# Kernel tuning notes

Hardware: AMD Instinct MI355X
Metric: run time of the kernel (lower is better)

## Reference

```python
import jax, jax.numpy as jnp
import numpy as np

BETA = 0.25  # commitment-loss weight


def setup_inputs() -> dict:
    key = jax.random.key(0)
    k1, k2 = jax.random.split(key)
    # x: [B, H, W, D] so that x.reshape(-1, D) groups per-pixel latent vectors
    x = jax.random.normal(k1, (32, 64, 64, 64), dtype=jnp.float32)
    # codebook: [D, K] as in the torch module (embedding_dim, num_embeddings)
    embedding = jax.random.normal(k2, (64, 1024), dtype=jnp.float32)
    return {"x": x, "embedding": embedding}


def reference(x, embedding):
    D, K = embedding.shape
    flat = x.reshape(-1, D)  # [N, D]
    # pairwise squared distances: ||z||^2 + ||e||^2 - 2 z.e  -> [N, K]
    distances = (
        jnp.sum(flat * flat, axis=1, keepdims=True)
        + jnp.sum(embedding * embedding, axis=0)
        - 2.0 * (flat @ embedding)
    )
    encoding_indices = jnp.argmin(distances, axis=1)  # [N]
    encodings = jax.nn.one_hot(encoding_indices, K, dtype=x.dtype)  # [N, K]
    # gather codewords (same math as encodings @ embedding.T, but O(N*D))
    quantized = jnp.take(embedding, encoding_indices, axis=1).T.reshape(x.shape)
    e_latent_loss = jnp.mean((jax.lax.stop_gradient(quantized) - x) ** 2)
    loss = BETA * e_latent_loss
    # straight-through estimator
    quantized_st = x + jax.lax.stop_gradient(quantized - x)
    avg_probs = jnp.mean(encodings, axis=0)
    perplexity = jnp.exp(-jnp.sum(avg_probs * jnp.log(avg_probs + 1e-10)))
    return quantized_st, loss, perplexity, encodings, encoding_indices
```

## Files before the change

### kernel.cpp

```cpp
#include <hip/hip_runtime.h>
#include <hip/hip_fp16.h>
#include <math.h>

#define NPIX    131072
#define DDIM    64
#define KCODE   1024
#define BETA    0.25f
#define EPS2    4e-3f
#define FIXCAP  2048
#define TAILROW 130944

#define Q_OFF    0
#define LOSS_OFF 8388608
#define PERP_OFF 8388609
#define ENC_OFF  8388610
#define IDX_OFF  142606338

#define TAIL_F     134086656
#define EHT_F      (TAIL_F + 2)
#define ELT_F      (TAIL_F + 32770)
#define FIXLIST_I  (TAIL_F + 65540)
#define FIXDELTA_F (TAIL_F + 69638)
#define FIXCOUNT_I (TAIL_F + 71688)


typedef _Float16 half8 __attribute__((ext_vector_type(8)));
typedef float    f32x4 __attribute__((ext_vector_type(4)));

__global__ void vq_prep(const float* __restrict__ emb, float* __restrict__ embT,
                        _Float16* __restrict__ eh, _Float16* __restrict__ el,
                        float* __restrict__ norms) {
    int b = blockIdx.x;
    if (b < 256) {
        int i = b * 256 + threadIdx.x;
        int d = i >> 10;
        int k = i & 1023;
        float v = emb[i];
        embT[k * DDIM + d] = v;
        _Float16 h = (_Float16)v;
        eh[k * DDIM + d] = h;
        el[k * DDIM + d] = (_Float16)(v - (float)h);
    } else {
        int k = (b - 256) * 256 + threadIdx.x;
        float s = 0.f;
        #pragma unroll 8
        for (int d = 0; d < DDIM; ++d) {
            float v = emb[d * KCODE + k];
            s = fmaf(v, v, s);
        }
        norms[k] = s;
    }
}

__global__ __launch_bounds__(256) void vq_argmin_fused(
        const float* __restrict__ x, const _Float16* __restrict__ eh,
        const _Float16* __restrict__ el, const float* __restrict__ norms,
        const float* __restrict__ embT, float* __restrict__ idxf,
        float* __restrict__ q, float* __restrict__ enc,
        int* __restrict__ hist, float* __restrict__ lossp,
        int* __restrict__ fixlist, int* __restrict__ fixcount) {
    __shared__ char lds_raw[33280];
    half8* EH8 = (half8*)lds_raw;
    half8* EL8 = (half8*)(lds_raw + 16384);
    float* NRM = (float*)(lds_raw + 32768);

    const int tid   = threadIdx.x;
    const int blkid = blockIdx.x;
    const int wave  = tid >> 6;
    const int lane  = tid & 63;
    const int lx = lane & 15;
    const int lk = lane >> 4;
    const int pixbase = blkid * 128 + wave * 32;

    half8 ah[2][2], al[2][2];
    float xp0 = 0.f, xp1 = 0.f;
    #pragma unroll
    for (int mt = 0; mt < 2; ++mt) {
        const float* xr = x + (size_t)(pixbase + mt * 16 + lx) * DDIM + lk * 8;
        float xps = 0.f;
        #pragma unroll
        for (int kh = 0; kh < 2; ++kh) {
            float4 v0 = *(const float4*)(xr + kh * 32);
            float4 v1 = *(const float4*)(xr + kh * 32 + 4);
            xps = fmaf(v0.x, v0.x, xps); xps = fmaf(v0.y, v0.y, xps);
            xps = fmaf(v0.z, v0.z, xps); xps = fmaf(v0.w, v0.w, xps);
            xps = fmaf(v1.x, v1.x, xps); xps = fmaf(v1.y, v1.y, xps);
            xps = fmaf(v1.z, v1.z, xps); xps = fmaf(v1.w, v1.w, xps);
            half8 hh, ll;
            float vv;
            vv = v0.x; hh[0] = (_Float16)vv; ll[0] = (_Float16)(vv - (float)hh[0]);
            vv = v0.y; hh[1] = (_Float16)vv; ll[1] = (_Float16)(vv - (float)hh[1]);
            vv = v0.z; hh[2] = (_Float16)vv; ll[2] = (_Float16)(vv - (float)hh[2]);
            vv = v0.w; hh[3] = (_Float16)vv; ll[3] = (_Float16)(vv - (float)hh[3]);
            vv = v1.x; hh[4] = (_Float16)vv; ll[4] = (_Float16)(vv - (float)hh[4]);
            vv = v1.y; hh[5] = (_Float16)vv; ll[5] = (_Float16)(vv - (float)hh[5]);
            vv = v1.z; hh[6] = (_Float16)vv; ll[6] = (_Float16)(vv - (float)hh[6]);
            vv = v1.w; hh[7] = (_Float16)vv; ll[7] = (_Float16)(vv - (float)hh[7]);
            ah[mt][kh] = hh;
            al[mt][kh] = ll;
        }
        if (mt == 0) xp0 = xps; else xp1 = xps;
    }
    float xn0 = xp0 + __shfl_xor(xp0, 16); xn0 += __shfl_xor(xn0, 32);
    float xn1 = xp1 + __shfl_xor(xp1, 16); xn1 += __shfl_xor(xn1, 32);

    float b1[2][4], b2[2][4];
    int   i1[2][4];
    #pragma unroll
    for (int mt = 0; mt < 2; ++mt)
        #pragma unroll
        for (int r = 0; r < 4; ++r) { b1[mt][r] = 3.4e38f; b2[mt][r] = 3.4e38f; i1[mt][r] = 0; }

    float* encB = enc + (size_t)blkid * 131072;
    f32x4* zb = (f32x4*)(encB + 2);

    #pragma unroll 1
    for (int t = 0; t < 8; ++t) {
        const int kbase = t * 128;
        __syncthreads();
        {
            const float4* sh = (const float4*)(eh + (size_t)kbase * DDIM);
            const float4* sl = (const float4*)(el + (size_t)kbase * DDIM);
            float4* dh = (float4*)EH8;
            float4* dl = (float4*)EL8;
            #pragma unroll
            for (int i = 0; i < 4; ++i) {
                int G = tid + i * 256;
                int code = G >> 3, g = G & 7;
                int sw = g ^ (code & 7);
                dh[code * 8 + sw] = sh[G];
                dl[code * 8 + sw] = sl[G];
            }
            if (tid < 128) NRM[tid] = norms[kbase + tid];
        }
        __syncthreads();

        #pragma unroll 1
        for (int c = 0; c < 8; ++c) {
            int code = c * 16 + lx;
            const half8* bhp = EH8 + code * 8;
            const half8* blp = EL8 + code * 8;
            int sw0 = lk ^ (code & 7);
            int sw1 = (lk + 4) ^ (code & 7);
            half8 bh0 = bhp[sw0], bh1 = bhp[sw1];
            half8 bl0 = blp[sw0], bl1 = blp[sw1];

            f32x4 acc0 = {0.f, 0.f, 0.f, 0.f};
            f32x4 acc1 = {0.f, 0.f, 0.f, 0.f};
            acc0 = __builtin_amdgcn_mfma_f32_16x16x32_f16(ah[0][0], bh0, acc0, 0, 0, 0);
            acc1 = __builtin_amdgcn_mfma_f32_16x16x32_f16(ah[1][0], bh0, acc1, 0, 0, 0);
            acc0 = __builtin_amdgcn_mfma_f32_16x16x32_f16(ah[0][1], bh1, acc0, 0, 0, 0);
            acc1 = __builtin_amdgcn_mfma_f32_16x16x32_f16(ah[1][1], bh1, acc1, 0, 0, 0);
            acc0 = __builtin_amdgcn_mfma_f32_16x16x32_f16(ah[0][0], bl0, acc0, 0, 0, 0);
            acc1 = __builtin_amdgcn_mfma_f32_16x16x32_f16(ah[1][0], bl0, acc1, 0, 0, 0);
            acc0 = __builtin_amdgcn_mfma_f32_16x16x32_f16(ah[0][1], bl1, acc0, 0, 0, 0);
            acc1 = __builtin_amdgcn_mfma_f32_16x16x32_f16(ah[1][1], bl1, acc1, 0, 0, 0);
            acc0 = __builtin_amdgcn_mfma_f32_16x16x32_f16(al[0][0], bh0, acc0, 0, 0, 0);
            acc1 = __builtin_amdgcn_mfma_f32_16x16x32_f16(al[1][0], bh0, acc1, 0, 0, 0);
            acc0 = __builtin_amdgcn_mfma_f32_16x16x32_f16(al[0][1], bh1, acc0, 0, 0, 0);
            acc1 = __builtin_amdgcn_mfma_f32_16x16x32_f16(al[1][1], bh1, acc1, 0, 0, 0);

            float nrm = NRM[c * 16 + lx];
            int codeg = kbase + c * 16 + lx;
            #pragma unroll
            for (int r = 0; r < 4; ++r) {
                float d0 = fmaf(-2.0f, acc0[r], nrm);
                bool lt0 = d0 < b1[0][r];
                b2[0][r] = fminf(b2[0][r], fmaxf(b1[0][r], d0));
                b1[0][r] = fminf(b1[0][r], d0);
                i1[0][r] = lt0 ? codeg : i1[0][r];
                float d1 = fmaf(-2.0f, acc1[r], nrm);
                bool lt1 = d1 < b1[1][r];
                b2[1][r] = fminf(b2[1][r], fmaxf(b1[1][r], d1));
                b1[1][r] = fminf(b1[1][r], d1);
                i1[1][r] = lt1 ? codeg : i1[1][r];
            }
        }

        if (blkid != 1023) {
            f32x4 z = {0.f, 0.f, 0.f, 0.f};
            #pragma unroll
            for (int it = 0; it < 16; ++it) {
                int fi = t * 4096 + it * 256 + tid;
                if (fi < 32767) zb[fi] = z;
            }
            if (t == 7 && tid == 0) {
                encB[0] = 0.f; encB[1] = 0.f;
                encB[131070] = 0.f; encB[131071] = 0.f;
            }
        }
    }

    __syncthreads();
    float* S  = (float*)(lds_raw + wave * 6528);
    float* SB1 = S, *SI = S + 544, *SB2 = S + 1088;
    int* idx_lds = (int*)(lds_raw + 26112);
    #pragma unroll
    for (int mt = 0; mt < 2; ++mt)
        #pragma unroll
        for (int r = 0; r < 4; ++r) {
            int p = mt * 16 + lk * 4 + r;
            SB1[p * 17 + lx] = b1[mt][r];
            SI [p * 17 + lx] = (float)i1[mt][r];
            SB2[p * 17 + lx] = b2[mt][r];
        }
    __syncthreads();

    float xf0 = __shfl(xn0, lane & 15);
    float xf1 = __shfl(xn1, lane & 15);
    float xf  = (lane >> 4) ? xf1 : xf0;

    float gb1 = 3.4e38f, gb2 = 3.4e38f;
    int gi1 = 0;
    if (lane < 32) {
        gi1 = KCODE;
        #pragma unroll
        for (int j = 0; j < 16; ++j) {
            float cb1 = SB1[lane * 17 + j];
            int   ci1 = (int)SI[lane * 17 + j];
            float cb2 = SB2[lane * 17 + j];
            if (cb1 < gb1 || (cb1 == gb1 && ci1 < gi1)) {
                gb2 = fminf(gb1, cb2); gb1 = cb1; gi1 = ci1;
            } else {
                gb2 = fminf(gb2, cb1);
            }
        }
        int pixel = pixbase + lane;
        idxf[pixel] = (float)gi1;
        idx_lds[wave * 32 + lane] = gi1;
        atomicAdd(&hist[gi1], 1);
        if (blkid != 1023) enc[(size_t)pixel * 1024 + gi1] = 1.f;
        if (gb2 - gb1 < EPS2) {
            int slot = atomicAdd(fixcount, 1);
            if (slot < FIXCAP) {
                fixlist[2 * slot]     = pixel;
                fixlist[2 * slot + 1] = __float_as_int(gb1);
            }
        }
    }

    float sq = (lane < 32) ? (gb1 + xf) : 0.f;
    #pragma unroll
    for (int m = 1; m < 64; m <<= 1) sq += __shfl_xor(sq, m);
    if (lane == 0) lossp[blkid * 4 + wave] = sq;

    __syncthreads();
    const f32x4* eT4 = (const f32x4*)embT;
    f32x4* q4 = (f32x4*)q;
    #pragma unroll
    for (int it = 0; it < 8; ++it) {
        int i = it * 256 + tid;
        int r = i >> 4, j = i & 15;
        int idx = idx_lds[r];
        q4[((size_t)blkid * 128 + r) * 16 + j] = eT4[idx * 16 + j];
    }
}

__global__ __launch_bounds__(64) void vq_fixup(
        const float* __restrict__ x, const float* __restrict__ embT,
        const float* __restrict__ norms, const int* __restrict__ fixlist,
        const int* __restrict__ fixcount, float* __restrict__ idxf,
        float* __restrict__ q, float* __restrict__ enc,
        int* __restrict__ hist, float* __restrict__ fixdelta) {
    int cnt = *fixcount;
    if (cnt > FIXCAP) cnt = FIXCAP;
    int b = blockIdx.x;
    if (b >= cnt) return;
    int pixel = fixlist[2 * b];
    float b1old = __int_as_float(fixlist[2 * b + 1]);
    int lane = threadIdx.x;

    float xr[64];
    const float4* x4 = (const float4*)(x + (size_t)pixel * DDIM);
    #pragma unroll
    for (int j = 0; j < 16; ++j) {
        float4 v = x4[j];
        xr[j * 4] = v.x; xr[j * 4 + 1] = v.y; xr[j * 4 + 2] = v.z; xr[j * 4 + 3] = v.w;
    }
    float bd = 3.4e38f;
    int bi = 0;
    #pragma unroll 1
    for (int c = 0; c < 16; ++c) {
        int k = lane * 16 + c;
        const float4* e4 = (const float4*)(embT + (size_t)k * DDIM);
        float a0 = 0.f, a1 = 0.f, a2 = 0.f, a3 = 0.f;
        #pragma unroll
        for (int j = 0; j < 16; ++j) {
            float4 ev = e4[j];
            a0 = fmaf(xr[j * 4],     ev.x, a0);
            a1 = fmaf(xr[j * 4 + 1], ev.y, a1);
            a2 = fmaf(xr[j * 4 + 2], ev.z, a2);
            a3 = fmaf(xr[j * 4 + 3], ev.w, a3);
        }
        float dd = fmaf(-2.0f, (a0 + a1) + (a2 + a3), norms[k]);
        if (dd < bd) { bd = dd; bi = k; }
    }
    #pragma unroll
    for (int m = 1; m < 64; m <<= 1) {
        float od = __shfl_xor(bd, m, 64);
        int   oi = __shfl_xor(bi, m, 64);
        if (od < bd || (od == bd && oi < bi)) { bd = od; bi = oi; }
    }
    q[(size_t)pixel * DDIM + lane] = embT[(size_t)bi * DDIM + lane];
    if (lane == 0) {
        int old = (int)idxf[pixel];
        idxf[pixel] = (float)bi;
        fixdelta[b] = bd - b1old;
        if (bi != old) {
            atomicAdd(&hist[old], -1);
            atomicAdd(&hist[bi], 1);
            if (pixel < TAILROW) {
                enc[(size_t)pixel * 1024 + old] = 0.f;
                enc[(size_t)pixel * 1024 + bi]  = 1.f;
            }
        }
    }
}

__global__ void vq_tail(const float* __restrict__ idxf, float* __restrict__ enc) {
    int r = blockIdx.x;
    int pixel = TAILROW + r;
    int idx = (int)idxf[pixel];
    size_t base = (size_t)pixel * 1024;
    int t = threadIdx.x;
    if (t < 255) {
        int k = 4 * t + 2;
        f32x4 v;
        v.x = (k     == idx) ? 1.f : 0.f;
        v.y = (k + 1 == idx) ? 1.f : 0.f;
        v.z = (k + 2 == idx) ? 1.f : 0.f;
        v.w = (k + 3 == idx) ? 1.f : 0.f;
        *(f32x4*)(enc + base + k) = v;
    } else {
        enc[base]        = (idx == 0)    ? 1.f : 0.f;
        enc[base + 1]    = (idx == 1)    ? 1.f : 0.f;
        enc[base + 1022] = (idx == 1022) ? 1.f : 0.f;
        enc[base + 1023] = (idx == 1023) ? 1.f : 0.f;
    }
}

__global__ void vq_final(const float* __restrict__ lossp, const int* __restrict__ hist,
                         const float* __restrict__ fixdelta,
                         const int* __restrict__ fixcount,
                         float* __restrict__ out_loss, float* __restrict__ out_perp) {
    __shared__ double red[256];
    int tid = threadIdx.x;
    double s = 0.0;
    for (int i = tid; i < 4096; i += 256) s += (double)lossp[i];
    red[tid] = s;
    __syncthreads();
    for (int st = 128; st > 0; st >>= 1) {
        if (tid < st) red[tid] += red[tid + st];
        __syncthreads();
    }
    if (tid == 0) {
        int cnt = *fixcount;
        if (cnt > FIXCAP) cnt = FIXCAP;
        double d = red[0];
        for (int i = 0; i < cnt; ++i) d += (double)fixdelta[i];
        *out_loss = (float)((double)BETA * d / (double)((size_t)NPIX * DDIM));
    }
    __syncthreads();

    double e = 0.0;
    for (int i = tid; i < KCODE; i += 256) {
        float p = (float)hist[i] / (float)NPIX;
        e += (double)(p * logf(p + 1e-10f));
    }
    red[tid] = e;
    __syncthreads();
    for (int st = 128; st > 0; st >>= 1) {
        if (tid < st) red[tid] += red[tid + st];
        __syncthreads();
    }
    if (tid == 0) *out_perp = expf((float)(-red[0]));
}

extern "C" void kernel_launch(void* const* d_in, const int* in_sizes, int n_in,
                              void* d_out, int out_size, void* d_ws, size_t ws_size,
                              hipStream_t stream) {
    const float* x   = (const float*)d_in[0];
    const float* emb = (const float*)d_in[1];
    float* out = (float*)d_out;

    char* ws = (char*)d_ws;
    float* lossp = (float*)ws;
    int*   hist  = (int*)(ws + 32768);
    float* norms = (float*)(ws + 36864);
    float* embT  = (float*)(ws + 40960);

    float* q      = out + Q_OFF;
    float* o_loss = out + LOSS_OFF;
    float* o_perp = out + PERP_OFF;
    float* enc    = out + ENC_OFF;
    float* idxf   = out + IDX_OFF;

    _Float16* eh    = (_Float16*)(enc + EHT_F);
    _Float16* el    = (_Float16*)(enc + ELT_F);
    int* fixlist    = (int*)(enc + FIXLIST_I);
    float* fixdelta = (float*)(enc + FIXDELTA_F);
    int* fixcount   = (int*)(enc + FIXCOUNT_I);

    (void)hipMemsetAsync(ws + 32768, 0, 4096, stream);
    (void)hipMemsetAsync((void*)fixcount, 0, 4, stream);

    vq_prep<<<260, 256, 0, stream>>>(emb, embT, eh, el, norms);
    vq_argmin_fused<<<1024, 256, 0, stream>>>(x, eh, el, norms, embT, idxf, q,
                                              enc, hist, lossp, fixlist, fixcount);
    vq_fixup<<<FIXCAP, 64, 0, stream>>>(x, embT, norms, fixlist, fixcount,
                                        idxf, q, enc, hist, fixdelta);
    vq_tail<<<128, 256, 0, stream>>>(idxf, enc);
    vq_final<<<1, 256, 0, stream>>>(lossp, hist, fixdelta, fixcount, o_loss, o_perp);
}
```

Before: 257.3 us.

## Stream pre-swizzled codebook panels into LDS via global_load_lds and overlap with zero-fill

The prep kernel now writes the fp16 hi/lo codebook already in the swizzled per-panel LDS layout, so the argmin kernel can copy each 128-code panel with direct global-to-LDS loads instead of register round-trips. The one-hot zero-fill stores are moved ahead of the compute, issued while the LDS loads are in flight, with manual waitcnt and raw s_barrier replacing one __syncthreads per panel. All 1024 norms are loaded into LDS once up front. This relies on hand-tuned vmcnt counts and sched barriers, which are fragile if the compiler reorders or changes the number of outstanding loads.

```diff
diff --git a/kernel.cpp b/kernel.cpp
--- a/kernel.cpp
+++ b/kernel.cpp
@@ -17,8 +17,8 @@
 #define IDX_OFF  142606338
 
 #define TAIL_F     134086656
-#define EHT_F      (TAIL_F + 2)
-#define ELT_F      (TAIL_F + 32770)
+#define EHS_F      (TAIL_F + 2)
+#define ELS_F      (TAIL_F + 32770)
 #define FIXLIST_I  (TAIL_F + 65540)
 #define FIXDELTA_F (TAIL_F + 69638)
 #define FIXCOUNT_I (TAIL_F + 71688)
@@ -26,9 +26,11 @@
 
 typedef _Float16 half8 __attribute__((ext_vector_type(8)));
 typedef float    f32x4 __attribute__((ext_vector_type(4)));
+typedef __attribute__((address_space(3))) void       lds_void_t;
+typedef __attribute__((address_space(1))) const void g_void_t;
 
 __global__ void vq_prep(const float* __restrict__ emb, float* __restrict__ embT,
-                        _Float16* __restrict__ eh, _Float16* __restrict__ el,
+                        _Float16* __restrict__ ehs, _Float16* __restrict__ els,
                         float* __restrict__ norms) {
     int b = blockIdx.x;
     if (b < 256) {
@@ -38,8 +40,12 @@
         float v = emb[i];
         embT[k * DDIM + d] = v;
         _Float16 h = (_Float16)v;
-        eh[k * DDIM + d] = h;
-        el[k * DDIM + d] = (_Float16)(v - (float)h);
+        _Float16 l = (_Float16)(v - (float)h);
+        int panel = k >> 7, codeP = k & 127;
+        int sw = (d >> 3) ^ (k & 7);
+        int fi = panel * 8192 + codeP * 64 + sw * 8 + (d & 7);
+        ehs[fi] = h;
+        els[fi] = l;
     } else {
         int k = (b - 256) * 256 + threadIdx.x;
         float s = 0.f;
@@ -53,16 +59,16 @@
 }
 
 __global__ __launch_bounds__(256) void vq_argmin_fused(
-        const float* __restrict__ x, const _Float16* __restrict__ eh,
-        const _Float16* __restrict__ el, const float* __restrict__ norms,
+        const float* __restrict__ x, const _Float16* __restrict__ ehs,
+        const _Float16* __restrict__ els, const float* __restrict__ norms,
         const float* __restrict__ embT, float* __restrict__ idxf,
         float* __restrict__ q, float* __restrict__ enc,
         int* __restrict__ hist, float* __restrict__ lossp,
         int* __restrict__ fixlist, int* __restrict__ fixcount) {
-    __shared__ char lds_raw[33280];
-    half8* EH8 = (half8*)lds_raw;
-    half8* EL8 = (half8*)(lds_raw + 16384);
-    float* NRM = (float*)(lds_raw + 32768);
+    __shared__ __align__(16) char lds_raw[36864];
+    half8* EH8   = (half8*)lds_raw;
+    half8* EL8   = (half8*)(lds_raw + 16384);
+    float* NRMa  = (float*)(lds_raw + 32768);
 
     const int tid   = threadIdx.x;
     const int blkid = blockIdx.x;
@@ -71,6 +77,9 @@
     const int lx = lane & 15;
     const int lk = lane >> 4;
     const int pixbase = blkid * 128 + wave * 32;
+
+    #pragma unroll
+    for (int i = 0; i < 4; ++i) NRMa[tid + i * 256] = norms[tid + i * 256];
 
     half8 ah[2][2], al[2][2];
     float xp0 = 0.f, xp1 = 0.f;
@@ -114,27 +123,43 @@
     float* encB = enc + (size_t)blkid * 131072;
     f32x4* zb = (f32x4*)(encB + 2);
 
+    __syncthreads();
+
     #pragma unroll 1
     for (int t = 0; t < 8; ++t) {
-        const int kbase = t * 128;
-        __syncthreads();
+        __builtin_amdgcn_sched_barrier(0);
+        __builtin_amdgcn_s_barrier();
+        __builtin_amdgcn_sched_barrier(0);
         {
-            const float4* sh = (const float4*)(eh + (size_t)kbase * DDIM);
-            const float4* sl = (const float4*)(el + (size_t)kbase * DDIM);
-            float4* dh = (float4*)EH8;
-            float4* dl = (float4*)EL8;
+            const char* gH = (const char*)ehs + (t << 14) + (tid << 4);
+            const char* gL = (const char*)els + (t << 14) + (tid << 4);
+            char* lH = &lds_raw[wave << 10];
+            char* lL = &lds_raw[16384 + (wave << 10)];
             #pragma unroll
             for (int i = 0; i < 4; ++i) {
-                int G = tid + i * 256;
-                int code = G >> 3, g = G & 7;
-                int sw = g ^ (code & 7);
-                dh[code * 8 + sw] = sh[G];
-                dl[code * 8 + sw] = sl[G];
-            }
-            if (tid < 128) NRM[tid] = norms[kbase + tid];
-        }
-        __syncthreads();
-
+                __builtin_amdgcn_global_load_lds((g_void_t*)(gH + (i << 12)),
+                                                 (lds_void_t*)(lH + (i << 12)), 16, 0, 0);
+                __builtin_amdgcn_global_load_lds((g_void_t*)(gL + (i << 12)),
+                                                 (lds_void_t*)(lL + (i << 12)), 16, 0, 0);
+            }
+        }
+        __builtin_amdgcn_sched_barrier(0);
+        if (blkid != 1023) {
+            f32x4 z = {0.f, 0.f, 0.f, 0.f};
+            #pragma unroll
+            for (int it = 0; it < 16; ++it) {
+                int fi = t * 4096 + it * 256 + tid;
+                if (fi < 32767) zb[fi] = z;
+            }
+            asm volatile("s_waitcnt vmcnt(16)" ::: "memory");
+        } else {
+            asm volatile("s_waitcnt vmcnt(0)" ::: "memory");
+        }
+        __builtin_amdgcn_sched_barrier(0);
+        __builtin_amdgcn_s_barrier();
+        __builtin_amdgcn_sched_barrier(0);
+
+        const int kbase = t * 128;
         #pragma unroll 1
         for (int c = 0; c < 8; ++c) {
             int code = c * 16 + lx;
@@ -160,7 +185,7 @@
             acc0 = __builtin_amdgcn_mfma_f32_16x16x32_f16(al[0][1], bh1, acc0, 0, 0, 0);
             acc1 = __builtin_amdgcn_mfma_f32_16x16x32_f16(al[1][1], bh1, acc1, 0, 0, 0);
 
-            float nrm = NRM[c * 16 + lx];
+            float nrm = NRMa[kbase + c * 16 + lx];
             int codeg = kbase + c * 16 + lx;
             #pragma unroll
             for (int r = 0; r < 4; ++r) {
@@ -176,22 +201,16 @@
                 i1[1][r] = lt1 ? codeg : i1[1][r];
             }
         }
-
-        if (blkid != 1023) {
-            f32x4 z = {0.f, 0.f, 0.f, 0.f};
-            #pragma unroll
-            for (int it = 0; it < 16; ++it) {
-                int fi = t * 4096 + it * 256 + tid;
-                if (fi < 32767) zb[fi] = z;
-            }
-            if (t == 7 && tid == 0) {
-                encB[0] = 0.f; encB[1] = 0.f;
-                encB[131070] = 0.f; encB[131071] = 0.f;
-            }
-        }
-    }
-
-    __syncthreads();
+        __builtin_amdgcn_sched_barrier(0);
+    }
+
+    if (blkid != 1023 && tid == 0) {
+        encB[0] = 0.f; encB[1] = 0.f;
+        encB[131070] = 0.f; encB[131071] = 0.f;
+    }
+    asm volatile("s_waitcnt vmcnt(0)" ::: "memory");
+    __syncthreads();
+
     float* S  = (float*)(lds_raw + wave * 6528);
     float* SB1 = S, *SI = S + 544, *SB2 = S + 1088;
     int* idx_lds = (int*)(lds_raw + 26112);
@@ -315,6 +334,43 @@
             }
         }
     }
+}
+
+__global__ void vq_final(const float* __restrict__ lossp, const int* __restrict__ hist,
+                         const float* __restrict__ fixdelta,
+                         const int* __restrict__ fixcount,
+                         float* __restrict__ out_loss, float* __restrict__ out_perp) {
+    __shared__ double red[256];
+    int tid = threadIdx.x;
+    double s = 0.0;
+    for (int i = tid; i < 4096; i += 256) s += (double)lossp[i];
+    red[tid] = s;
+    __syncthreads();
+    for (int st = 128; st > 0; st >>= 1) {
+        if (tid < st) red[tid] += red[tid + st];
+        __syncthreads();
+    }
+    if (tid == 0) {
+        int cnt = *fixcount;
+        if (cnt > FIXCAP) cnt = FIXCAP;
+        double d = red[0];
+        for (int i = 0; i < cnt; ++i) d += (double)fixdelta[i];
+        *out_loss = (float)((double)BETA * d / (double)((size_t)NPIX * DDIM));
+    }
+    __syncthreads();
+
+    double e = 0.0;
+    for (int i = tid; i < KCODE; i += 256) {
+        float p = (float)hist[i] / (float)NPIX;
+        e += (double)(p * logf(p + 1e-10f));
+    }
+    red[tid] = e;
+    __syncthreads();
+    for (int st = 128; st > 0; st >>= 1) {
+        if (tid < st) red[tid] += red[tid + st];
+        __syncthreads();
+    }
+    if (tid == 0) *out_perp = expf((float)(-red[0]));
 }
 
 __global__ void vq_tail(const float* __restrict__ idxf, float* __restrict__ enc) {
@@ -339,43 +395,6 @@
     }
 }
 
-__global__ void vq_final(const float* __restrict__ lossp, const int* __restrict__ hist,
-                         const float* __restrict__ fixdelta,
-                         const int* __restrict__ fixcount,
-                         float* __restrict__ out_loss, float* __restrict__ out_perp) {
-    __shared__ double red[256];
-    int tid = threadIdx.x;
-    double s = 0.0;
-    for (int i = tid; i < 4096; i += 256) s += (double)lossp[i];
-    red[tid] = s;
-    __syncthreads();
-    for (int st = 128; st > 0; st >>= 1) {
-        if (tid < st) red[tid] += red[tid + st];
-        __syncthreads();
-    }
-    if (tid == 0) {
-        int cnt = *fixcount;
-        if (cnt > FIXCAP) cnt = FIXCAP;
-        double d = red[0];
-        for (int i = 0; i < cnt; ++i) d += (double)fixdelta[i];
-        *out_loss = (float)((double)BETA * d / (double)((size_t)NPIX * DDIM));
-    }
-    __syncthreads();
-
-    double e = 0.0;
-    for (int i = tid; i < KCODE; i += 256) {
-        float p = (float)hist[i] / (float)NPIX;
-        e += (double)(p * logf(p + 1e-10f));
-    }
-    red[tid] = e;
-    __syncthreads();
-    for (int st = 128; st > 0; st >>= 1) {
-        if (tid < st) red[tid] += red[tid + st];
-        __syncthreads();
-    }
-    if (tid == 0) *out_perp = expf((float)(-red[0]));
-}
-
 extern "C" void kernel_launch(void* const* d_in, const int* in_sizes, int n_in,
                               void* d_out, int out_size, void* d_ws, size_t ws_size,
                               hipStream_t stream) {
@@ -395,8 +414,8 @@
     float* enc    = out + ENC_OFF;
     float* idxf   = out + IDX_OFF;
 
-    _Float16* eh    = (_Float16*)(enc + EHT_F);
-    _Float16* el    = (_Float16*)(enc + ELT_F);
+    _Float16* ehs   = (_Float16*)(enc + EHS_F);
+    _Float16* els   = (_Float16*)(enc + ELS_F);
     int* fixlist    = (int*)(enc + FIXLIST_I);
     float* fixdelta = (float*)(enc + FIXDELTA_F);
     int* fixcount   = (int*)(enc + FIXCOUNT_I);
@@ -404,11 +423,11 @@
     (void)hipMemsetAsync(ws + 32768, 0, 4096, stream);
     (void)hipMemsetAsync((void*)fixcount, 0, 4, stream);
 
-    vq_prep<<<260, 256, 0, stream>>>(emb, embT, eh, el, norms);
-    vq_argmin_fused<<<1024, 256, 0, stream>>>(x, eh, el, norms, embT, idxf, q,
+    vq_prep<<<260, 256, 0, stream>>>(emb, embT, ehs, els, norms);
+    vq_argmin_fused<<<1024, 256, 0, stream>>>(x, ehs, els, norms, embT, idxf, q,
                                               enc, hist, lossp, fixlist, fixcount);
     vq_fixup<<<FIXCAP, 64, 0, stream>>>(x, embT, norms, fixlist, fixcount,
                                         idxf, q, enc, hist, fixdelta);
+    vq_final<<<1, 256, 0, stream>>>(lossp, hist, fixdelta, fixcount, o_loss, o_perp);
     vq_tail<<<128, 256, 0, stream>>>(idxf, enc);
-    vq_final<<<1, 256, 0, stream>>>(lossp, hist, fixdelta, fixcount, o_loss, o_perp);
-}
+}
```

Measured after the change: 206.5 us, median of 2. 19.7% less time.
